# Kernel optimization log

Measured on AMD Instinct MI355X. Metric: run time of the kernel, lower is better.

## Reference

```python
import jax, jax.numpy as jnp
import numpy as np

N = 100000          # num_nodes
E = 1_600_000       # num_edges
F = 16              # node_features
HID = 32            # DCRNN hidden size (hardcoded in DCRNNModel)
OUT = 12            # output_len
K = 2               # diffusion steps (intended DCRNN; see notes)
CIN = F + HID       # DConv input channels: concat([X, H])


def setup_inputs() -> dict:
    key = jax.random.key(0)
    ks = jax.random.split(key, 12)
    x = jax.random.normal(ks[0], (N, F), dtype=jnp.float32)
    edge_index = jax.random.randint(ks[1], (2, E), 0, N, dtype=jnp.int32)
    edge_weight = jax.random.uniform(ks[2], (E,), jnp.float32, minval=0.05, maxval=1.0)
    sc = 0.1
    W_z = jax.random.normal(ks[3], (2, K, CIN, HID), jnp.float32) * sc
    b_z = jax.random.normal(ks[4], (HID,), jnp.float32) * sc
    W_r = jax.random.normal(ks[5], (2, K, CIN, HID), jnp.float32) * sc
    b_r = jax.random.normal(ks[6], (HID,), jnp.float32) * sc
    W_h = jax.random.normal(ks[7], (2, K, CIN, HID), jnp.float32) * sc
    b_h = jax.random.normal(ks[8], (HID,), jnp.float32) * sc
    lin_W = jax.random.normal(ks[9], (HID, OUT), jnp.float32) * sc
    lin_b = jax.random.normal(ks[10], (OUT,), jnp.float32) * sc
    return {"x": x, "edge_index": edge_index, "edge_weight": edge_weight,
            "W_z": W_z, "b_z": b_z, "W_r": W_r, "b_r": b_r,
            "W_h": W_h, "b_h": b_h, "lin_W": lin_W, "lin_b": lin_b}


def reference(x, edge_index, edge_weight, W_z, b_z, W_r, b_r, W_h, b_h, lin_W, lin_b):
    src, dst = edge_index[0], edge_index[1]
    # weighted out/in degrees (as in to_dense_adj row/col sums)
    deg_out = jax.ops.segment_sum(edge_weight, src, num_segments=N)
    deg_in = jax.ops.segment_sum(edge_weight, dst, num_segments=N)
    inv_out_e = (1.0 / deg_out)[src][:, None]  # [E,1] per-edge 1/deg_out(src)
    inv_in_e = (1.0 / deg_in)[dst][:, None]    # [E,1] per-edge 1/deg_in(dst)

    def dconv(Xc, W, b):
        # K=0 term (both diffusion directions share Tx_0 = X)
        H = Xc @ W[0, 0] + Xc @ W[1, 0]
        # forward diffusion: out[dst] += (1/deg_out[src]) * Xc[src]
        T_o = jax.ops.segment_sum(inv_out_e * Xc[src], dst, num_segments=N)
        # reverse diffusion: out[src] += (1/deg_in[dst]) * Xc[dst]
        T_i = jax.ops.segment_sum(inv_in_e * Xc[dst], src, num_segments=N)
        return H + T_o @ W[0, 1] + T_i @ W[1, 1] + b

    H0 = jnp.zeros((N, HID), dtype=x.dtype)
    XH = jnp.concatenate([x, H0], axis=1)           # [N, F+HID]
    Z = jax.nn.sigmoid(dconv(XH, W_z, b_z))         # update gate
    R = jax.nn.sigmoid(dconv(XH, W_r, b_r))         # reset gate
    XHr = jnp.concatenate([x, H0 * R], axis=1)
    H_tilde = jnp.tanh(dconv(XHr, W_h, b_h))
    H = Z * H0 + (1.0 - Z) * H_tilde                # [N, HID]
    return jax.nn.relu(H) @ lin_W + lin_b           # [N, OUT]
```

## Files before the change

kernel.cpp:

```cpp
#include <hip/hip_runtime.h>
#include <math.h>

#define N_NODES 100000
#define N_EDGES 1600000
#define NF 16
#define HID 32
#define OUTD 12
#define CIN3 48

#define NB   1024
#define RNG  98
#define PBLK 256
#define PT   1024
#define CHUNK ((N_EDGES + PBLK - 1) / PBLK)
#define CAP   2560
#define CAPT  10
#define ACCN  7

typedef unsigned int uint;


__global__ __launch_bounds__(PT)
void p1_count(const int* __restrict__ ei, uint* __restrict__ cntD, uint* __restrict__ cntS) {
    __shared__ uint cD[NB], cS[NB];
    int t = threadIdx.x, blk = blockIdx.x;
    for (int i = t; i < NB; i += PT) { cD[i] = 0; cS[i] = 0; }
    __syncthreads();
    int lo = blk * CHUNK, hi = min(lo + CHUNK, N_EDGES);
    for (int e = lo + t; e < hi; e += PT) {
        uint s = (uint)ei[e];
        uint d = (uint)ei[N_EDGES + e];
        atomicAdd(&cS[s / RNG], 1u);
        atomicAdd(&cD[d / RNG], 1u);
    }
    __syncthreads();
    for (int i = t; i < NB; i += PT) {
        cntD[i * PBLK + blk] = cD[i];
        cntS[i * PBLK + blk] = cS[i];
    }
}

__global__ __launch_bounds__(256)
void p2a_rowsum(const uint* __restrict__ cntD, const uint* __restrict__ cntS,
                uint* __restrict__ totD, uint* __restrict__ totS) {
    __shared__ uint red[256];
    int t = threadIdx.x;
    bool isS = blockIdx.x >= NB;
    int b = isS ? (blockIdx.x - NB) : blockIdx.x;
    const uint* cnt = isS ? cntS : cntD;
    red[t] = cnt[b * PBLK + t];
    __syncthreads();
    for (int s = 128; s > 0; s >>= 1) { if (t < s) red[t] += red[t + s]; __syncthreads(); }
    if (t == 0) (isS ? totS : totD)[b] = red[0];
}

__global__ __launch_bounds__(256)
void p2b_scan(const uint* __restrict__ totD, const uint* __restrict__ totS,
              uint* __restrict__ baseD, uint* __restrict__ baseS) {
    __shared__ uint part[256];
    int t = threadIdx.x;
    for (int dir = 0; dir < 2; ++dir) {
        const uint* tot = dir ? totS : totD;
        uint* base = dir ? baseS : baseD;
        uint v[4]; uint s = 0;
#pragma unroll
        for (int k = 0; k < 4; ++k) { v[k] = tot[t * 4 + k]; s += v[k]; }
        part[t] = s;
        __syncthreads();
        if (t == 0) {
            uint a = 0;
            for (int k = 0; k < 256; ++k) { uint x = part[k]; part[k] = a; a += x; }
            base[NB] = a;
        }
        __syncthreads();
        uint a = part[t];
#pragma unroll
        for (int k = 0; k < 4; ++k) { base[t * 4 + k] = a; a += v[k]; }
        __syncthreads();
    }
}

__global__ __launch_bounds__(256)
void p2c_rowscan(const uint* __restrict__ cntD, const uint* __restrict__ cntS,
                 const uint* __restrict__ baseD, const uint* __restrict__ baseS,
                 uint* __restrict__ offD, uint* __restrict__ offS) {
    __shared__ uint row[PBLK];
    int t = threadIdx.x;
    bool isS = blockIdx.x >= NB;
    int b = isS ? (blockIdx.x - NB) : blockIdx.x;
    const uint* cnt = isS ? cntS : cntD;
    const uint* base = isS ? baseS : baseD;
    uint* off = isS ? offS : offD;
    row[t] = cnt[b * PBLK + t];
    __syncthreads();
    if (t == 0) {
        uint a = base[b];
        for (int k = 0; k < PBLK; ++k) { uint v = row[k]; row[k] = a; a += v; }
    }
    __syncthreads();
    off[b * PBLK + t] = row[t];
}

__global__ __launch_bounds__(PT)
void p3_scatter(const int* __restrict__ ei, const float* __restrict__ ew,
                const uint* __restrict__ offD, const uint* __restrict__ offS,
                uint2* __restrict__ recD, uint2* __restrict__ recS) {
    __shared__ uint curD[NB], curS[NB];
    int t = threadIdx.x, blk = blockIdx.x;
    for (int b = t; b < NB; b += PT) {
        curD[b] = offD[b * PBLK + blk];
        curS[b] = offS[b * PBLK + blk];
    }
    __syncthreads();
    int lo = blk * CHUNK, hi = min(lo + CHUNK, N_EDGES);
    for (int e = lo + t; e < hi; e += PT) {
        uint s = (uint)ei[e];
        uint d = (uint)ei[N_EDGES + e];
        uint wfix = (uint)(ew[e] * 16777216.0f + 0.5f);
        uint bd = d / RNG, dl = d - bd * RNG;
        uint p = atomicAdd(&curD[bd], 1u);
        recD[p] = make_uint2(s | (dl << 20), (dl << 25) | wfix);
        uint bs = s / RNG, sl = s - bs * RNG;
        uint p2 = atomicAdd(&curS[bs], 1u);
        recS[p2] = make_uint2(d | (sl << 20), (sl << 25) | wfix);
    }
}

__global__ __launch_bounds__(256)
void kdeg(const uint2* __restrict__ recD, const uint2* __restrict__ recS,
          const uint* __restrict__ baseD, const uint* __restrict__ baseS,
          float* __restrict__ inv_in, float* __restrict__ inv_out) {
    __shared__ uint dacc[RNG];
    int t = threadIdx.x;
    bool isS = blockIdx.x >= NB;
    int b = isS ? (blockIdx.x - NB) : blockIdx.x;
    const uint2* rec = isS ? recS : recD;
    const uint* base = isS ? baseS : baseD;
    float* inv = isS ? inv_out : inv_in;
    for (int i = t; i < RNG; i += 256) dacc[i] = 0u;
    __syncthreads();
    uint lo = base[b], hi = base[b + 1];
    for (uint e = lo + t; e < hi; e += 256) {
        uint ry = rec[e].y;
        atomicAdd(&dacc[ry >> 25], ry & 0x1FFFFFFu);
    }
    __syncthreads();
    int n0 = b * RNG;
    for (int i = t; i < RNG; i += 256) {
        int n = n0 + i;
        if (n < N_NODES) inv[n] = 16777216.0f / (float)dacc[i];
    }
}

__global__ __launch_bounds__(256)
void p4_sorted(const uint2* __restrict__ recD, const uint2* __restrict__ recS,
               const uint* __restrict__ baseD, const uint* __restrict__ baseS,
               const float* __restrict__ x,
               const float* __restrict__ inv_out, const float* __restrict__ inv_in,
               float* __restrict__ To, float* __restrict__ Ti) {
    __shared__ uint sorted[CAP];
    __shared__ uint scnt[RNG];
    __shared__ uint cstart[RNG + 1];
    __shared__ uint scur[RNG];
    int t = threadIdx.x;
    bool isS = blockIdx.x >= NB;
    int b = isS ? (blockIdx.x - NB) : blockIdx.x;
    const uint2* rec = isS ? recS : recD;
    const uint* base = isS ? baseS : baseD;
    const float* inv = isS ? inv_in : inv_out;
    float* out = isS ? Ti : To;

    int f = t & 15, s = t >> 4;
    uint lo = base[b], hi = base[b + 1];

    float acc[ACCN];
#pragma unroll
    for (int k = 0; k < ACCN; ++k) acc[k] = 0.0f;

    for (uint chunk = lo; chunk < hi; chunk += CAP) {
        uint n_in = min(hi - chunk, (uint)CAP);
        for (int i = t; i < RNG; i += 256) scnt[i] = 0;
        __syncthreads();
        uint stash[CAPT];
#pragma unroll
        for (int k = 0; k < CAPT; ++k) {
            uint i = (uint)(k * 256 + t);
            if (i < n_in) {
                uint r = rec[chunk + i].x;
                stash[k] = r;
                atomicAdd(&scnt[r >> 20], 1u);
            }
        }
        __syncthreads();
        if (t == 0) {
            uint a = 0;
            for (int n = 0; n < RNG; ++n) { cstart[n] = a; a += scnt[n]; }
            cstart[RNG] = a;
        }
        __syncthreads();
        for (int i = t; i < RNG; i += 256) scur[i] = cstart[i];
        __syncthreads();
#pragma unroll
        for (int k = 0; k < CAPT; ++k) {
            uint i = (uint)(k * 256 + t);
            if (i < n_in) {
                uint r = stash[k];
                uint p = atomicAdd(&scur[r >> 20], 1u);
                sorted[p] = r;
            }
        }
        __syncthreads();
#pragma unroll
        for (int k = 0; k < ACCN; ++k) {
            int n = s + 16 * k;
            if (n < RNG) {
                uint j = cstart[n], j1 = cstart[n + 1];
                for (; j + 8 <= j1; j += 8) {
                    uint p0 = sorted[j],     p1 = sorted[j + 1], p2 = sorted[j + 2], p3 = sorted[j + 3];
                    uint p4 = sorted[j + 4], p5 = sorted[j + 5], p6 = sorted[j + 6], p7 = sorted[j + 7];
                    uint o0 = p0 & 0xFFFFFu, o1 = p1 & 0xFFFFFu, o2 = p2 & 0xFFFFFu, o3 = p3 & 0xFFFFFu;
                    uint o4 = p4 & 0xFFFFFu, o5 = p5 & 0xFFFFFu, o6 = p6 & 0xFFFFFu, o7 = p7 & 0xFFFFFu;
                    float g0 = x[(size_t)o0 * NF + f], g1 = x[(size_t)o1 * NF + f];
                    float g2 = x[(size_t)o2 * NF + f], g3 = x[(size_t)o3 * NF + f];
                    float g4 = x[(size_t)o4 * NF + f], g5 = x[(size_t)o5 * NF + f];
                    float g6 = x[(size_t)o6 * NF + f], g7 = x[(size_t)o7 * NF + f];
                    float w0 = inv[o0], w1 = inv[o1], w2 = inv[o2], w3 = inv[o3];
                    float w4 = inv[o4], w5 = inv[o5], w6 = inv[o6], w7 = inv[o7];
                    acc[k] += g0 * w0 + g1 * w1 + g2 * w2 + g3 * w3
                            + g4 * w4 + g5 * w5 + g6 * w6 + g7 * w7;
                }
                for (; j < j1; ++j) {
                    uint p = sorted[j];
                    uint o = p & 0xFFFFFu;
                    acc[k] += x[(size_t)o * NF + f] * inv[o];
                }
            }
        }
        __syncthreads();
    }

#pragma unroll
    for (int k = 0; k < ACCN; ++k) {
        int n = s + 16 * k;
        if (n < RNG) {
            size_t g = (size_t)b * RNG + n;
            if (g < N_NODES) out[g * NF + f] = acc[k];
        }
    }
}

__global__ void wprep_kernel(const float* __restrict__ Wz, const float* __restrict__ Wh,
                             float* __restrict__ WzT, float* __restrict__ WhT) {
    int t = blockIdx.x * blockDim.x + threadIdx.x;
    if (t >= 2 * CIN3 * HID) return;
    const float* W = (t < CIN3 * HID) ? Wz : Wh;
    float* WT      = (t < CIN3 * HID) ? WzT : WhT;
    int i = (t < CIN3 * HID) ? t : (t - CIN3 * HID);
    int c = i / HID;
    int h = i - c * HID;
    float v;
    if (c < 16)      v = W[(0 * 48 + c) * 32 + h] + W[(2 * 48 + c) * 32 + h];
    else if (c < 32) v = W[(1 * 48 + (c - 16)) * 32 + h];
    else             v = W[(3 * 48 + (c - 32)) * 32 + h];
    WT[h * CIN3 + c] = v;
}

__global__ __launch_bounds__(256)
void node_kernel(const float* __restrict__ x, const float* __restrict__ To,
                 const float* __restrict__ Ti,
                 const float* __restrict__ WzT, const float* __restrict__ WhT,
                 const float* __restrict__ bz, const float* __restrict__ bh,
                 const float* __restrict__ linW, const float* __restrict__ linb,
                 float* __restrict__ out) {
    __shared__ __align__(16) float sWz[HID * CIN3];
    __shared__ __align__(16) float sWh[HID * CIN3];
    __shared__ __align__(16) float sBz[HID], sBh[HID];
    __shared__ __align__(16) float sLW[HID * OUTD];
    __shared__ __align__(16) float sLb[OUTD];

    for (int i = threadIdx.x; i < HID * CIN3; i += 256) { sWz[i] = WzT[i]; sWh[i] = WhT[i]; }
    if (threadIdx.x < HID) { sBz[threadIdx.x] = bz[threadIdx.x]; sBh[threadIdx.x] = bh[threadIdx.x]; }
    for (int i = threadIdx.x; i < HID * OUTD; i += 256) sLW[i] = linW[i];
    if (threadIdx.x < OUTD) sLb[threadIdx.x] = linb[threadIdx.x];
    __syncthreads();

    int n = blockIdx.x * 256 + threadIdx.x;
    if (n >= N_NODES) return;

    float feat[CIN3];
#pragma unroll
    for (int q = 0; q < 4; ++q) {
        float4 v = ((const float4*)(x + (size_t)n * NF))[q];
        feat[q*4+0]=v.x; feat[q*4+1]=v.y; feat[q*4+2]=v.z; feat[q*4+3]=v.w;
    }
#pragma unroll
    for (int q = 0; q < 4; ++q) {
        float4 v = ((const float4*)(To + (size_t)n * NF))[q];
        feat[16+q*4+0]=v.x; feat[16+q*4+1]=v.y; feat[16+q*4+2]=v.z; feat[16+q*4+3]=v.w;
    }
#pragma unroll
    for (int q = 0; q < 4; ++q) {
        float4 v = ((const float4*)(Ti + (size_t)n * NF))[q];
        feat[32+q*4+0]=v.x; feat[32+q*4+1]=v.y; feat[32+q*4+2]=v.z; feat[32+q*4+3]=v.w;
    }

    float o[OUTD];
#pragma unroll
    for (int j = 0; j < OUTD; ++j) o[j] = sLb[j];

#pragma unroll 2
    for (int h = 0; h < HID; ++h) {
        float az = sBz[h];
        float ah = sBh[h];
        const float4* wz4 = (const float4*)(sWz + h * CIN3);
        const float4* wh4 = (const float4*)(sWh + h * CIN3);
#pragma unroll
        for (int q = 0; q < CIN3 / 4; ++q) {
            float4 wz = wz4[q];
            float4 wh = wh4[q];
            float f0 = feat[q*4+0], f1 = feat[q*4+1], f2 = feat[q*4+2], f3 = feat[q*4+3];
            az += f0*wz.x + f1*wz.y + f2*wz.z + f3*wz.w;
            ah += f0*wh.x + f1*wh.y + f2*wh.z + f3*wh.w;
        }
        float z  = 1.0f / (1.0f + expf(-az));
        float ht = tanhf(ah);
        float r  = fmaxf((1.0f - z) * ht, 0.0f);
#pragma unroll
        for (int j = 0; j < OUTD; ++j) o[j] += r * sLW[h * OUTD + j];
    }

    float4* op = (float4*)(out + (size_t)n * OUTD);
    op[0] = make_float4(o[0], o[1], o[2],  o[3]);
    op[1] = make_float4(o[4], o[5], o[6],  o[7]);
    op[2] = make_float4(o[8], o[9], o[10], o[11]);
}

__global__ void zero_kernel(float* __restrict__ p, int n) {
    int i = blockIdx.x * blockDim.x + threadIdx.x;
    int stride = gridDim.x * blockDim.x;
    for (; i < n; i += stride) p[i] = 0.0f;
}
__global__ void degree_compact(const int* __restrict__ ei, const float* __restrict__ ew,
                               float* __restrict__ deg_out, float* __restrict__ deg_in) {
    int e = blockIdx.x * blockDim.x + threadIdx.x;
    if (e >= N_EDGES) return;
    atomicAdd(&deg_out[ei[e]], ew[e]);
    atomicAdd(&deg_in[ei[N_EDGES + e]], ew[e]);
}
__global__ void rcp_compact(float* __restrict__ a, float* __restrict__ b) {
    int n = blockIdx.x * blockDim.x + threadIdx.x;
    if (n >= N_NODES) return;
    a[n] = 1.0f / a[n]; b[n] = 1.0f / b[n];
}
__global__ __launch_bounds__(256)
void scatter_kernel(const int* __restrict__ ei, const float* __restrict__ x,
                    const float* __restrict__ inv_out, const float* __restrict__ inv_in,
                    float* __restrict__ To, float* __restrict__ Ti) {
    int t = blockIdx.x * blockDim.x + threadIdx.x;
    if (t >= N_EDGES * NF) return;
    int e = t >> 4, f = t & 15;
    int src = ei[e], dst = ei[N_EDGES + e];
    atomicAdd(&To[dst * NF + f], x[src * NF + f] * inv_out[src]);
    atomicAdd(&Ti[src * NF + f], x[dst * NF + f] * inv_in[dst]);
}

extern "C" void kernel_launch(void* const* d_in, const int* in_sizes, int n_in,
                              void* d_out, int out_size, void* d_ws, size_t ws_size,
                              hipStream_t stream) {
    const float* x    = (const float*)d_in[0];
    const int*   ei   = (const int*)  d_in[1];
    const float* ew   = (const float*)d_in[2];
    const float* Wz   = (const float*)d_in[3];
    const float* bz   = (const float*)d_in[4];
    const float* Wh   = (const float*)d_in[7];
    const float* bh   = (const float*)d_in[8];
    const float* linW = (const float*)d_in[9];
    const float* linb = (const float*)d_in[10];

    float* ws = (float*)d_ws;

    size_t off = 0;
    uint2* recD = (uint2*)(ws + off); off += 2 * (size_t)N_EDGES;
    uint2* recS = (uint2*)(ws + off); off += 2 * (size_t)N_EDGES;
    uint* cntD  = (uint*)(ws + off);  off += (size_t)NB * PBLK;
    uint* cntS  = (uint*)(ws + off);  off += (size_t)NB * PBLK;
    uint* offD  = (uint*)(ws + off);  off += (size_t)NB * PBLK;
    uint* offS  = (uint*)(ws + off);  off += (size_t)NB * PBLK;
    uint* totD  = (uint*)(ws + off);  off += NB;
    uint* totS  = (uint*)(ws + off);  off += NB;
    uint* baseD = (uint*)(ws + off);  off += NB + 1;
    uint* baseS = (uint*)(ws + off);  off += NB + 1;
    float* inv_out = ws + off;        off += N_NODES;
    float* inv_in  = ws + off;        off += N_NODES;
    float* To   = ws + off;           off += (size_t)NF * N_NODES;
    float* Ti   = ws + off;           off += (size_t)NF * N_NODES;
    float* WzT  = ws + off;           off += CIN3 * HID;
    float* WhT  = ws + off;           off += CIN3 * HID;
    size_t need = off * sizeof(float);

    if (ws_size >= need) {
        p1_count    <<<PBLK,  PT,  0, stream>>>(ei, cntD, cntS);
        p2a_rowsum  <<<2*NB,  256, 0, stream>>>(cntD, cntS, totD, totS);
        p2b_scan    <<<1,     256, 0, stream>>>(totD, totS, baseD, baseS);
        p2c_rowscan <<<2*NB,  256, 0, stream>>>(cntD, cntS, baseD, baseS, offD, offS);
        p3_scatter  <<<PBLK,  PT,  0, stream>>>(ei, ew, offD, offS, recD, recS);
        kdeg        <<<2*NB,  256, 0, stream>>>(recD, recS, baseD, baseS, inv_in, inv_out);
        wprep_kernel<<<12,    256, 0, stream>>>(Wz, Wh, WzT, WhT);
        p4_sorted   <<<2*NB,  256, 0, stream>>>(recD, recS, baseD, baseS, x, inv_out, inv_in, To, Ti);
        node_kernel <<<(N_NODES + 255) / 256, 256, 0, stream>>>(x, To, Ti, WzT, WhT, bz, bh,
                                                                linW, linb, (float*)d_out);
    } else {
        float* fTo  = ws;
        float* fTi  = ws + 16 * N_NODES;
        float* fIo  = ws + 32 * N_NODES;
        float* fIi  = ws + 33 * N_NODES;
        float* fWzT = ws + 34 * N_NODES;
        float* fWhT = fWzT + CIN3 * HID;
        zero_kernel<<<2048, 256, 0, stream>>>(fTo, 34 * N_NODES);
        degree_compact<<<(N_EDGES + 255) / 256, 256, 0, stream>>>(ei, ew, fIo, fIi);
        rcp_compact<<<(N_NODES + 255) / 256, 256, 0, stream>>>(fIo, fIi);
        scatter_kernel<<<(N_EDGES * NF + 255) / 256, 256, 0, stream>>>(ei, x, fIo, fIi, fTo, fTi);
        wprep_kernel<<<12, 256, 0, stream>>>(Wz, Wh, fWzT, fWhT);
        node_kernel<<<(N_NODES + 255) / 256, 256, 0, stream>>>(x, fTo, fTi, fWzT, fWhT, bz, bh,
                                                               linW, linb, (float*)d_out);
    }
}
```

Before: 156.0 us.

## Locally sort edges by bucket in shared memory before scattering records

The scatter kernel now handles each direction separately. It first counting-sorts the block's edge chunk by destination bucket in shared memory, using a histogram, a Hillis-Steele scan and atomic placement, and then writes the records in bucket order. Consecutive threads therefore write to contiguous global positions, which replaces the earlier fully random scattered writes and should make global stores more coalesced. In exchange the edge arrays are read several times, extra shared-memory scans and barriers are added, and shared-memory use grows, which may lower occupancy.

```diff
diff --git a/kernel.cpp b/kernel.cpp
--- a/kernel.cpp
+++ b/kernel.cpp
@@ -105,24 +105,58 @@
 void p3_scatter(const int* __restrict__ ei, const float* __restrict__ ew,
                 const uint* __restrict__ offD, const uint* __restrict__ offS,
                 uint2* __restrict__ recD, uint2* __restrict__ recS) {
-    __shared__ uint curD[NB], curS[NB];
+    __shared__ uint sorted[CHUNK];
+    __shared__ uint scnt[NB];
+    __shared__ uint sbuf[NB];
+    __shared__ uint cstart[NB + 1];
+    __shared__ uint scur[NB];
     int t = threadIdx.x, blk = blockIdx.x;
-    for (int b = t; b < NB; b += PT) {
-        curD[b] = offD[b * PBLK + blk];
-        curS[b] = offS[b * PBLK + blk];
-    }
-    __syncthreads();
     int lo = blk * CHUNK, hi = min(lo + CHUNK, N_EDGES);
-    for (int e = lo + t; e < hi; e += PT) {
-        uint s = (uint)ei[e];
-        uint d = (uint)ei[N_EDGES + e];
-        uint wfix = (uint)(ew[e] * 16777216.0f + 0.5f);
-        uint bd = d / RNG, dl = d - bd * RNG;
-        uint p = atomicAdd(&curD[bd], 1u);
-        recD[p] = make_uint2(s | (dl << 20), (dl << 25) | wfix);
-        uint bs = s / RNG, sl = s - bs * RNG;
-        uint p2 = atomicAdd(&curS[bs], 1u);
-        recS[p2] = make_uint2(d | (sl << 20), (sl << 25) | wfix);
+    int n = hi - lo;
+
+    for (int dir = 0; dir < 2; ++dir) {
+        const uint* off = dir ? offS : offD;
+        uint2* rec      = dir ? recS : recD;
+        const int* own  = dir ? ei : (ei + N_EDGES);
+        scnt[t] = 0;
+        __syncthreads();
+        for (int i = t; i < n; i += PT)
+            atomicAdd(&scnt[(uint)own[lo + i] / RNG], 1u);
+        __syncthreads();
+        uint v = scnt[t];
+        sbuf[t] = v;
+        __syncthreads();
+        for (int d = 1; d < NB; d <<= 1) {
+            uint a = (t >= d) ? sbuf[t - d] : 0u;
+            __syncthreads();
+            sbuf[t] += a;
+            __syncthreads();
+        }
+        cstart[t] = sbuf[t] - v;
+        scur[t]   = sbuf[t] - v;
+        if (t == 0) cstart[NB] = (uint)n;
+        __syncthreads();
+        sbuf[t] = off[t * PBLK + blk];
+        for (int i = t; i < n; i += PT) {
+            uint b = (uint)own[lo + i] / RNG;
+            uint p = atomicAdd(&scur[b], 1u);
+            sorted[p] = (b << 13) | (uint)i;
+        }
+        __syncthreads();
+        for (int i = t; i < n; i += PT) {
+            uint v2 = sorted[i];
+            uint b = v2 >> 13;
+            int e = lo + (int)(v2 & 8191u);
+            uint s  = (uint)ei[e];
+            uint d2 = (uint)ei[N_EDGES + e];
+            uint wfix = (uint)(ew[e] * 16777216.0f + 0.5f);
+            uint ownode = dir ? s : d2;
+            uint other  = dir ? d2 : s;
+            uint lcl  = ownode - b * RNG;
+            uint gpos = sbuf[b] + (i - cstart[b]);
+            rec[gpos] = make_uint2(other | (lcl << 20), (lcl << 25) | wfix);
+        }
+        __syncthreads();
     }
 }
 
```

New measurement: 163.0 us. 4.5% more time.
